# Kernel tuning notes

Hardware: AMD Instinct MI355X
Metric: run time of the kernel (lower is better)

The kernel has to match this reference:

```python
import jax, jax.numpy as jnp
import numpy as np

B, L, E, H = 2, 2048, 1024, 16
HD = E // H  # head_dim = 64
MASKED_BIAS = -10000.0


def setup_inputs() -> dict:
    key = jax.random.key(0)
    k0, k1, k2 = jax.random.split(key, 3)
    x = jax.random.normal(k0, (B, L, E), dtype=jnp.float32)
    attn_mask = jnp.zeros((B, 1, 1, L), dtype=jnp.float32)  # additive padding mask (0 = keep)
    W_in = jax.random.normal(k1, (E, 3 * E), dtype=jnp.float32) * (E ** -0.5)
    b_in = jnp.zeros((3 * E,), dtype=jnp.float32)
    W_out = jax.random.normal(k2, (E, E), dtype=jnp.float32) * (E ** -0.5)
    b_out = jnp.zeros((E,), dtype=jnp.float32)
    return {"x": x, "attn_mask": attn_mask, "W_in": W_in, "b_in": b_in,
            "W_out": W_out, "b_out": b_out}


def _split_heads(t):
    # [B, L, E] -> [B, H, L, HD]
    return t.reshape(B, L, H, HD).transpose(0, 2, 1, 3)


def reference(x, attn_mask, W_in, b_in, W_out, b_out):
    qkv = x @ W_in + b_in                      # [B, L, 3E]
    q, k, v = jnp.split(qkv, 3, axis=2)
    q, k, v = _split_heads(q), _split_heads(k), _split_heads(v)  # [B,H,L,HD]

    # Faithful to source: Q/K cast to bf16 before the score matmul.
    qb = q.astype(jnp.bfloat16)
    kb = k.astype(jnp.bfloat16)
    scores = jnp.einsum('bhqd,bhkd->bhqk', qb, kb)  # bf16 [B,H,L,L]
    scores = scores / float(HD) ** 0.5              # scale_attn_weights=True

    causal = jnp.tril(jnp.ones((L, L), dtype=bool))  # [L, L]
    scores = jnp.where(causal, scores, MASKED_BIAS)  # stays bf16
    # Adding the fp32 attn_mask promotes scores to fp32 (matches torch promotion).
    scores = scores + attn_mask                      # [B,H,L,L] fp32

    attn = jax.nn.softmax(scores, axis=-1)           # fp32, this is _attn_weights
    out = jnp.einsum('bhqk,bhkd->bhqd', attn, v)     # [B,H,L,HD]

    out = out.transpose(0, 2, 1, 3).reshape(B, L, E)  # merge heads
    out = out @ W_out + b_out                         # [B, L, E]
    return (out, attn)
```

## Files before the change

kernel.cpp:

```cpp
#include <hip/hip_runtime.h>


#define B_ 2
#define L_ 2048
#define E_ 1024
#define H_ 16
#define HD_ 64
#define M_FIX 16.0f

typedef __attribute__((ext_vector_type(8))) __bf16 bf16x8;
typedef __attribute__((ext_vector_type(4))) __bf16 bf16x4;
typedef __attribute__((ext_vector_type(4))) float f32x4;

typedef __attribute__((address_space(1))) const void gvoid_t;
typedef __attribute__((address_space(3))) void lvoid_t;

__device__ __forceinline__ void g2l16(const void* g, void* l) {
  __builtin_amdgcn_global_load_lds((gvoid_t*)g, (lvoid_t*)l, 16, 0, 0);
}

__device__ __forceinline__ f32x4 mfma16(bf16x8 a, bf16x8 b, f32x4 c) {
  return __builtin_amdgcn_mfma_f32_16x16x32_bf16(a, b, c, 0, 0, 0);
}

__global__ __launch_bounds__(256) void f32_to_bf16_vec(
    const float* __restrict__ in, __bf16* __restrict__ out, int n) {
  int i = (blockIdx.x * blockDim.x + threadIdx.x) * 4;
  if (i >= n) return;
  float4 v = *(const float4*)(in + i);
  bf16x4 o = {(__bf16)v.x, (__bf16)v.y, (__bf16)v.z, (__bf16)v.w};
  *(bf16x4*)(out + i) = o;
}

__global__ __launch_bounds__(256) void transpose_to_bf16(
    const float* __restrict__ in, __bf16* __restrict__ out, int R, int C) {
  __shared__ __bf16 tile[32][33];
  int c0 = blockIdx.x * 32, r0 = blockIdx.y * 32;
  int tx = threadIdx.x, ty = threadIdx.y;
  for (int i = ty; i < 32; i += 8)
    tile[i][tx] = (__bf16)in[(size_t)(r0 + i) * C + c0 + tx];
  __syncthreads();
  for (int i = ty; i < 32; i += 8)
    out[(size_t)(c0 + i) * R + r0 + tx] = tile[tx][i];
}

__global__ __launch_bounds__(256) void gemm_bf16_k(
    const __bf16* __restrict__ A, const __bf16* __restrict__ Bt,
    const float* __restrict__ bias, int M, int N, int K, int mode,
    float* __restrict__ outF, __bf16* __restrict__ Qb,
    __bf16* __restrict__ Kb, __bf16* __restrict__ Vt) {
  const f32x4 fz = {0.f, 0.f, 0.f, 0.f};
  int n0 = blockIdx.x * 128, m0 = blockIdx.y * 128;
  int w = threadIdx.x >> 6, l = threadIdx.x & 63;
  int wr = w >> 1, wc = w & 1, lr = l & 15, lg = l >> 4;
  __shared__ __bf16 Al[128 * 64];
  __shared__ __bf16 Bl[128 * 64];
  f32x4 acc[4][4];
#pragma unroll
  for (int i = 0; i < 4; ++i)
#pragma unroll
    for (int j = 0; j < 4; ++j) acc[i][j] = fz;

  for (int k0 = 0; k0 < K; k0 += 64) {
    __syncthreads();
#pragma unroll
    for (int i = 0; i < 4; ++i) {
      int base = (w * 4 + i) * 1024;
      int boff = base + l * 16;
      int row = boff >> 7, ch = (boff >> 4) & 7;
      g2l16(A + (size_t)(m0 + row) * K + k0 + ch * 8, (char*)Al + base);
      g2l16(Bt + (size_t)(n0 + row) * K + k0 + ch * 8, (char*)Bl + base);
    }
    __syncthreads();
    bf16x8 af[2][4], bfr[2][4];
#pragma unroll
    for (int ks = 0; ks < 2; ++ks)
#pragma unroll
      for (int f = 0; f < 4; ++f) {
        af[ks][f]  = *(const bf16x8*)&Al[(wr * 64 + f * 16 + lr) * 64 + ks * 32 + lg * 8];
        bfr[ks][f] = *(const bf16x8*)&Bl[(wc * 64 + f * 16 + lr) * 64 + ks * 32 + lg * 8];
      }
#pragma unroll
    for (int ks = 0; ks < 2; ++ks)
#pragma unroll
      for (int mf = 0; mf < 4; ++mf)
#pragma unroll
        for (int nf = 0; nf < 4; ++nf)
          acc[mf][nf] = mfma16(af[ks][mf], bfr[ks][nf], acc[mf][nf]);
  }

#pragma unroll
  for (int mf = 0; mf < 4; ++mf)
#pragma unroll
    for (int nf = 0; nf < 4; ++nf) {
      int ncol = n0 + wc * 64 + nf * 16 + lr;
      float bv = bias[ncol];
      int mr0 = m0 + wr * 64 + mf * 16 + lg * 4;
      if (mode == 1) {
#pragma unroll
        for (int jj = 0; jj < 4; ++jj)
          outF[(size_t)(mr0 + jj) * N + ncol] = acc[mf][nf][jj] + bv;
      } else {
        int reg = ncol >> 10, nn = ncol & 1023;
        int hh = nn >> 6, dd = nn & 63;
        int bb = mr0 >> 11, lp = mr0 & 2047;
        size_t bh = (size_t)bb * H_ + hh;
        if (reg == 2) {
          bf16x4 vv = {(__bf16)(acc[mf][nf][0] + bv), (__bf16)(acc[mf][nf][1] + bv),
                       (__bf16)(acc[mf][nf][2] + bv), (__bf16)(acc[mf][nf][3] + bv)};
          *(bf16x4*)&Vt[(bh * HD_ + dd) * L_ + lp] = vv;
        } else {
          __bf16* dst = (reg == 0) ? Qb : Kb;
#pragma unroll
          for (int jj = 0; jj < 4; ++jj)
            dst[(bh * L_ + lp + jj) * HD_ + dd] = (__bf16)(acc[mf][nf][jj] + bv);
        }
      }
    }
}

__global__ __launch_bounds__(256) void attn_fused3(
    const __bf16* __restrict__ Qb, const __bf16* __restrict__ Kb,
    const __bf16* __restrict__ Vt, const float* __restrict__ amask,
    float* __restrict__ attn_out, __bf16* __restrict__ merged) {
  const f32x4 fz = {0.f, 0.f, 0.f, 0.f};
  int id = blockIdx.x;
  int bh = id & 31;
  int qt = 15 - (id >> 5);
  int b = bh >> 4, h = bh & 15;
  int w = threadIdx.x >> 6, l = threadIdx.x & 63;
  int lr = l & 15, lg = l >> 4;
  const __bf16* Qh = Qb + (size_t)bh * L_ * HD_;
  const char* Kc = (const char*)(Kb + (size_t)bh * L_ * HD_);
  const char* Vc = (const char*)(Vt + (size_t)bh * HD_ * L_);
  float* attn = attn_out + (size_t)bh * L_ * L_;
  const float* mb = amask + (size_t)b * L_;

  __shared__ __bf16 Kl[2][64 * 64];
  __shared__ __bf16 Vl[2][64 * 64];
  __shared__ __bf16 Pl[4][32 * 64];
  __shared__ float Ml[L_];

  {
    int t = threadIdx.x;
    *(f32x4*)&Ml[t * 8] = *(const f32x4*)&mb[t * 8];
    *(f32x4*)&Ml[t * 8 + 4] = *(const f32x4*)&mb[t * 8 + 4];
  }

  int r0 = qt * 128 + w * 32 + lr;
  int r1 = r0 + 16;
  int ncc = 2 * qt + 2;

  bf16x8 qA0 = *(const bf16x8*)&Qh[(size_t)r0 * HD_ + lg * 8];
  bf16x8 qA1 = *(const bf16x8*)&Qh[(size_t)r0 * HD_ + 32 + lg * 8];
  bf16x8 qB0 = *(const bf16x8*)&Qh[(size_t)r1 * HD_ + lg * 8];
  bf16x8 qB1 = *(const bf16x8*)&Qh[(size_t)r1 * HD_ + 32 + lg * 8];

  auto stageK = [&](int c, int buf) {
#pragma unroll
    for (int i = 0; i < 2; ++i) {
      int seg = w * 2 + i;
      int grow = seg * 8 + (l >> 3);
      int sc8 = (l & 7) ^ (grow & 7);
      g2l16(Kc + (size_t)c * 8192 + grow * 128 + sc8 * 16,
            (char*)&Kl[buf][0] + seg * 1024);
    }
  };
  auto stageV = [&](int c, int buf) {
#pragma unroll
    for (int i = 0; i < 2; ++i) {
      int seg = w * 2 + i;
      int grow = seg * 8 + (l >> 3);
      int sc8 = (l & 7) ^ (grow & 7);
      g2l16(Vc + (size_t)grow * 4096 + (size_t)c * 128 + sc8 * 16,
            (char*)&Vl[buf][0] + seg * 1024);
    }
  };
  auto readS = [&](const __bf16* base, int row, int hf) -> bf16x8 {
    int c8 = (hf * 4 + lg) ^ (row & 7);
    return *(const bf16x8*)((const char*)base + row * 128 + c8 * 16);
  };
  auto writeP = [&](int ri, int cf, const bf16x4& v) {
    int c8 = (cf * 2 + (lg >> 1)) ^ (ri & 7);
    *(bf16x4*)((char*)&Pl[w][0] + ri * 128 + c8 * 16 + (lg & 1) * 8) = v;
  };
  auto readP = [&](int ri, int hf) -> bf16x8 {
    int c8 = (hf * 4 + lg) ^ (ri & 7);
    return *(const bf16x8*)((const char*)&Pl[w][0] + ri * 128 + c8 * 16);
  };

  float lA = 0.f, lB = 0.f;
  stageK(0, 0);
  __syncthreads();
  int cur = 0;
  for (int c = 0; c < ncc; ++c) {
    if (c + 1 < ncc) stageK(c + 1, cur ^ 1);
    f32x4 aA[4], aB[4];
#pragma unroll
    for (int cf = 0; cf < 4; ++cf) {
      bf16x8 k0 = readS(Kl[cur], cf * 16 + lr, 0);
      bf16x8 k1 = readS(Kl[cur], cf * 16 + lr, 1);
      aA[cf] = mfma16(k0, qA0, fz);
      aA[cf] = mfma16(k1, qA1, aA[cf]);
      aB[cf] = mfma16(k0, qB0, fz);
      aB[cf] = mfma16(k1, qB1, aB[cf]);
    }
    float sa = 0.f, sb = 0.f;
#pragma unroll
    for (int cf = 0; cf < 4; ++cf) {
      f32x4 mk = *(const f32x4*)&Ml[c * 64 + cf * 16 + lg * 4];
#pragma unroll
      for (int jj = 0; jj < 4; ++jj) {
        int col = c * 64 + cf * 16 + lg * 4 + jj;
        float svA = (float)(__bf16)aA[cf][jj] * 0.125f;
        if (col > r0) svA = -9984.0f;
        sa += __expf(svA + mk[jj] - M_FIX);
        float svB = (float)(__bf16)aB[cf][jj] * 0.125f;
        if (col > r1) svB = -9984.0f;
        sb += __expf(svB + mk[jj] - M_FIX);
      }
    }
    lA += sa;
    lB += sb;
    __syncthreads();
    cur ^= 1;
  }
  lA += __shfl_xor(lA, 16, 64);
  lA += __shfl_xor(lA, 32, 64);
  lB += __shfl_xor(lB, 16, 64);
  lB += __shfl_xor(lB, 32, 64);
  float liA = 1.0f / lA, liB = 1.0f / lB;

  f32x4 oA[4] = {fz, fz, fz, fz};
  f32x4 oB[4] = {fz, fz, fz, fz};
  stageK(0, 0);
  stageV(0, 0);
  __syncthreads();
  cur = 0;
  for (int c = 0; c < ncc; ++c) {
    if (c + 1 < ncc) {
      stageK(c + 1, cur ^ 1);
      stageV(c + 1, cur ^ 1);
    }
    asm volatile("" ::: "memory");
    f32x4 aA[4], aB[4];
#pragma unroll
    for (int cf = 0; cf < 4; ++cf) {
      bf16x8 k0 = readS(Kl[cur], cf * 16 + lr, 0);
      bf16x8 k1 = readS(Kl[cur], cf * 16 + lr, 1);
      aA[cf] = mfma16(k0, qA0, fz);
      aA[cf] = mfma16(k1, qA1, aA[cf]);
      aB[cf] = mfma16(k0, qB0, fz);
      aB[cf] = mfma16(k1, qB1, aB[cf]);
    }
#pragma unroll
    for (int cf = 0; cf < 4; ++cf) {
      f32x4 mk = *(const f32x4*)&Ml[c * 64 + cf * 16 + lg * 4];
      f32x4 pA, pB;
#pragma unroll
      for (int jj = 0; jj < 4; ++jj) {
        int col = c * 64 + cf * 16 + lg * 4 + jj;
        float svA = (float)(__bf16)aA[cf][jj] * 0.125f;
        if (col > r0) svA = -9984.0f;
        pA[jj] = __expf(svA + mk[jj] - M_FIX) * liA;
        float svB = (float)(__bf16)aB[cf][jj] * 0.125f;
        if (col > r1) svB = -9984.0f;
        pB[jj] = __expf(svB + mk[jj] - M_FIX) * liB;
      }
      *(f32x4*)&attn[(size_t)r0 * L_ + c * 64 + cf * 16 + lg * 4] = pA;
      *(f32x4*)&attn[(size_t)r1 * L_ + c * 64 + cf * 16 + lg * 4] = pB;
      bf16x4 ha = {(__bf16)pA[0], (__bf16)pA[1], (__bf16)pA[2], (__bf16)pA[3]};
      bf16x4 hb = {(__bf16)pB[0], (__bf16)pB[1], (__bf16)pB[2], (__bf16)pB[3]};
      writeP(lr, cf, ha);
      writeP(16 + lr, cf, hb);
    }
    bf16x8 pA0 = readP(lr, 0), pA1 = readP(lr, 1);
    bf16x8 pB0 = readP(16 + lr, 0), pB1 = readP(16 + lr, 1);
#pragma unroll
    for (int dt = 0; dt < 4; ++dt) {
      bf16x8 v0 = readS(Vl[cur], dt * 16 + lr, 0);
      bf16x8 v1 = readS(Vl[cur], dt * 16 + lr, 1);
      oA[dt] = mfma16(v0, pA0, oA[dt]);
      oA[dt] = mfma16(v1, pA1, oA[dt]);
      oB[dt] = mfma16(v0, pB0, oB[dt]);
      oB[dt] = mfma16(v1, pB1, oB[dt]);
    }
    asm volatile("s_waitcnt vmcnt(8)" ::: "memory");
    __builtin_amdgcn_s_barrier();
    __builtin_amdgcn_sched_barrier(0);
    cur ^= 1;
  }

#pragma unroll
  for (int dt = 0; dt < 4; ++dt) {
    bf16x4 oa = {(__bf16)oA[dt][0], (__bf16)oA[dt][1], (__bf16)oA[dt][2],
                 (__bf16)oA[dt][3]};
    bf16x4 ob = {(__bf16)oB[dt][0], (__bf16)oB[dt][1], (__bf16)oB[dt][2],
                 (__bf16)oB[dt][3]};
    *(bf16x4*)&merged[((size_t)b * L_ + r0) * E_ + h * HD_ + dt * 16 + lg * 4] = oa;
    *(bf16x4*)&merged[((size_t)b * L_ + r1) * E_ + h * HD_ + dt * 16 + lg * 4] = ob;
  }

  for (int c = ncc; c < 32; ++c)
#pragma unroll
    for (int q = 0; q < 4; ++q) {
      *(f32x4*)&attn[(size_t)r0 * L_ + c * 64 + q * 16 + lg * 4] = fz;
      *(f32x4*)&attn[(size_t)r1 * L_ + c * 64 + q * 16 + lg * 4] = fz;
    }
}

extern "C" void kernel_launch(void* const* d_in, const int* in_sizes, int n_in,
                              void* d_out, int out_size, void* d_ws,
                              size_t ws_size, hipStream_t stream) {
  const float* x     = (const float*)d_in[0];
  const float* amask = (const float*)d_in[1];
  const float* W_in  = (const float*)d_in[2];
  const float* b_in  = (const float*)d_in[3];
  const float* W_out = (const float*)d_in[4];
  const float* b_out = (const float*)d_in[5];

  float* out  = (float*)d_out;
  float* attn = out + (size_t)B_ * L_ * E_;

  char* ws = (char*)d_ws;
  __bf16* xb     = (__bf16*)(ws + 0);
  __bf16* WtIn   = (__bf16*)(ws + 8388608);
  __bf16* WtOut  = (__bf16*)(ws + 14680064);
  __bf16* Qb     = (__bf16*)(ws + 16777216);
  __bf16* Kb     = (__bf16*)(ws + 25165824);
  __bf16* Vt     = (__bf16*)(ws + 33554432);
  __bf16* merged = (__bf16*)(ws + 41943040);

  int nx = B_ * L_ * E_;
  f32_to_bf16_vec<<<nx / (256 * 4), 256, 0, stream>>>(x, xb, nx);
  transpose_to_bf16<<<dim3(3 * E_ / 32, E_ / 32), dim3(32, 8), 0, stream>>>(
      W_in, WtIn, E_, 3 * E_);
  transpose_to_bf16<<<dim3(E_ / 32, E_ / 32), dim3(32, 8), 0, stream>>>(
      W_out, WtOut, E_, E_);

  gemm_bf16_k<<<dim3(3 * E_ / 128, B_ * L_ / 128), 256, 0, stream>>>(
      xb, WtIn, b_in, B_ * L_, 3 * E_, E_, 0, nullptr, Qb, Kb, Vt);

  attn_fused3<<<16 * 32, 256, 0, stream>>>(Qb, Kb, Vt, amask, attn, merged);

  gemm_bf16_k<<<dim3(E_ / 128, B_ * L_ / 128), 256, 0, stream>>>(
      merged, WtOut, b_out, B_ * L_, E_, E_, 1, out, nullptr, nullptr,
      nullptr);
}
```

Measured before the change: 286.1 us.

## Split attention over key range into two halves and double-buffer GEMM staging

After: 330.5 us. +15.5%, slower.

```diff
diff --git a/kernel.cpp b/kernel.cpp
--- a/kernel.cpp
+++ b/kernel.cpp
@@ -53,32 +53,41 @@
   int n0 = blockIdx.x * 128, m0 = blockIdx.y * 128;
   int w = threadIdx.x >> 6, l = threadIdx.x & 63;
   int wr = w >> 1, wc = w & 1, lr = l & 15, lg = l >> 4;
-  __shared__ __bf16 Al[128 * 64];
-  __shared__ __bf16 Bl[128 * 64];
+  __shared__ __bf16 Al[2][128 * 64];
+  __shared__ __bf16 Bl[2][128 * 64];
   f32x4 acc[4][4];
 #pragma unroll
   for (int i = 0; i < 4; ++i)
 #pragma unroll
     for (int j = 0; j < 4; ++j) acc[i][j] = fz;
 
-  for (int k0 = 0; k0 < K; k0 += 64) {
-    __syncthreads();
+  auto stage = [&](int k0, int buf) {
 #pragma unroll
     for (int i = 0; i < 4; ++i) {
       int base = (w * 4 + i) * 1024;
       int boff = base + l * 16;
       int row = boff >> 7, ch = (boff >> 4) & 7;
-      g2l16(A + (size_t)(m0 + row) * K + k0 + ch * 8, (char*)Al + base);
-      g2l16(Bt + (size_t)(n0 + row) * K + k0 + ch * 8, (char*)Bl + base);
-    }
-    __syncthreads();
+      g2l16(A + (size_t)(m0 + row) * K + k0 + ch * 8, (char*)&Al[buf][0] + base);
+      g2l16(Bt + (size_t)(n0 + row) * K + k0 + ch * 8, (char*)&Bl[buf][0] + base);
+    }
+  };
+
+  int nk = K >> 6;
+  stage(0, 0);
+  asm volatile("s_waitcnt vmcnt(0)" ::: "memory");
+  __builtin_amdgcn_s_barrier();
+  __builtin_amdgcn_sched_barrier(0);
+  int cur = 0;
+  for (int t = 0; t < nk; ++t) {
+    if (t + 1 < nk) stage((t + 1) << 6, cur ^ 1);
+    asm volatile("" ::: "memory");
     bf16x8 af[2][4], bfr[2][4];
 #pragma unroll
     for (int ks = 0; ks < 2; ++ks)
 #pragma unroll
       for (int f = 0; f < 4; ++f) {
-        af[ks][f]  = *(const bf16x8*)&Al[(wr * 64 + f * 16 + lr) * 64 + ks * 32 + lg * 8];
-        bfr[ks][f] = *(const bf16x8*)&Bl[(wc * 64 + f * 16 + lr) * 64 + ks * 32 + lg * 8];
+        af[ks][f]  = *(const bf16x8*)&Al[cur][(wr * 64 + f * 16 + lr) * 64 + ks * 32 + lg * 8];
+        bfr[ks][f] = *(const bf16x8*)&Bl[cur][(wc * 64 + f * 16 + lr) * 64 + ks * 32 + lg * 8];
       }
 #pragma unroll
     for (int ks = 0; ks < 2; ++ks)
@@ -87,6 +96,10 @@
 #pragma unroll
         for (int nf = 0; nf < 4; ++nf)
           acc[mf][nf] = mfma16(af[ks][mf], bfr[ks][nf], acc[mf][nf]);
+    asm volatile("s_waitcnt vmcnt(0)" ::: "memory");
+    __builtin_amdgcn_s_barrier();
+    __builtin_amdgcn_sched_barrier(0);
+    cur ^= 1;
   }
 
 #pragma unroll
@@ -119,37 +132,27 @@
     }
 }
 
-__global__ __launch_bounds__(256) void attn_fused3(
+__global__ __launch_bounds__(256) void attn_p1(
     const __bf16* __restrict__ Qb, const __bf16* __restrict__ Kb,
-    const __bf16* __restrict__ Vt, const float* __restrict__ amask,
-    float* __restrict__ attn_out, __bf16* __restrict__ merged) {
+    const float* __restrict__ amask, float* __restrict__ lpart) {
   const f32x4 fz = {0.f, 0.f, 0.f, 0.f};
   int id = blockIdx.x;
   int bh = id & 31;
-  int qt = 15 - (id >> 5);
-  int b = bh >> 4, h = bh & 15;
+  int t = id >> 5;
+  int qt = 15 - (t >> 1);
+  int ph = t & 1;
+  int b = bh >> 4;
   int w = threadIdx.x >> 6, l = threadIdx.x & 63;
   int lr = l & 15, lg = l >> 4;
   const __bf16* Qh = Qb + (size_t)bh * L_ * HD_;
   const char* Kc = (const char*)(Kb + (size_t)bh * L_ * HD_);
-  const char* Vc = (const char*)(Vt + (size_t)bh * HD_ * L_);
-  float* attn = attn_out + (size_t)bh * L_ * L_;
   const float* mb = amask + (size_t)b * L_;
 
   __shared__ __bf16 Kl[2][64 * 64];
-  __shared__ __bf16 Vl[2][64 * 64];
-  __shared__ __bf16 Pl[4][32 * 64];
-  __shared__ float Ml[L_];
-
-  {
-    int t = threadIdx.x;
-    *(f32x4*)&Ml[t * 8] = *(const f32x4*)&mb[t * 8];
-    *(f32x4*)&Ml[t * 8 + 4] = *(const f32x4*)&mb[t * 8 + 4];
-  }
 
   int r0 = qt * 128 + w * 32 + lr;
   int r1 = r0 + 16;
-  int ncc = 2 * qt + 2;
+  int c0 = ph * (qt + 1), c1 = c0 + qt + 1;
 
   bf16x8 qA0 = *(const bf16x8*)&Qh[(size_t)r0 * HD_ + lg * 8];
   bf16x8 qA1 = *(const bf16x8*)&Qh[(size_t)r0 * HD_ + 32 + lg * 8];
@@ -166,35 +169,17 @@
             (char*)&Kl[buf][0] + seg * 1024);
     }
   };
-  auto stageV = [&](int c, int buf) {
-#pragma unroll
-    for (int i = 0; i < 2; ++i) {
-      int seg = w * 2 + i;
-      int grow = seg * 8 + (l >> 3);
-      int sc8 = (l & 7) ^ (grow & 7);
-      g2l16(Vc + (size_t)grow * 4096 + (size_t)c * 128 + sc8 * 16,
-            (char*)&Vl[buf][0] + seg * 1024);
-    }
-  };
   auto readS = [&](const __bf16* base, int row, int hf) -> bf16x8 {
     int c8 = (hf * 4 + lg) ^ (row & 7);
     return *(const bf16x8*)((const char*)base + row * 128 + c8 * 16);
   };
-  auto writeP = [&](int ri, int cf, const bf16x4& v) {
-    int c8 = (cf * 2 + (lg >> 1)) ^ (ri & 7);
-    *(bf16x4*)((char*)&Pl[w][0] + ri * 128 + c8 * 16 + (lg & 1) * 8) = v;
-  };
-  auto readP = [&](int ri, int hf) -> bf16x8 {
-    int c8 = (hf * 4 + lg) ^ (ri & 7);
-    return *(const bf16x8*)((const char*)&Pl[w][0] + ri * 128 + c8 * 16);
-  };
 
   float lA = 0.f, lB = 0.f;
-  stageK(0, 0);
+  stageK(c0, 0);
   __syncthreads();
   int cur = 0;
-  for (int c = 0; c < ncc; ++c) {
-    if (c + 1 < ncc) stageK(c + 1, cur ^ 1);
+  for (int c = c0; c < c1; ++c) {
+    if (c + 1 < c1) stageK(c + 1, cur ^ 1);
     f32x4 aA[4], aB[4];
 #pragma unroll
     for (int cf = 0; cf < 4; ++cf) {
@@ -208,7 +193,7 @@
     float sa = 0.f, sb = 0.f;
 #pragma unroll
     for (int cf = 0; cf < 4; ++cf) {
-      f32x4 mk = *(const f32x4*)&Ml[c * 64 + cf * 16 + lg * 4];
+      f32x4 mk = *(const f32x4*)&mb[c * 64 + cf * 16 + lg * 4];
 #pragma unroll
       for (int jj = 0; jj < 4; ++jj) {
         int col = c * 64 + cf * 16 + lg * 4 + jj;
@@ -229,16 +214,92 @@
   lA += __shfl_xor(lA, 32, 64);
   lB += __shfl_xor(lB, 16, 64);
   lB += __shfl_xor(lB, 32, 64);
-  float liA = 1.0f / lA, liB = 1.0f / lB;
+  if (lg == 0) {
+    lpart[ph * (B_ * H_ * L_) + bh * L_ + r0] = lA;
+    lpart[ph * (B_ * H_ * L_) + bh * L_ + r1] = lB;
+  }
+}
+
+__global__ __launch_bounds__(256) void attn_p2(
+    const __bf16* __restrict__ Qb, const __bf16* __restrict__ Kb,
+    const __bf16* __restrict__ Vt, const float* __restrict__ amask,
+    const float* __restrict__ lpart, float* __restrict__ attn_out,
+    __bf16* __restrict__ op0, __bf16* __restrict__ op1) {
+  const f32x4 fz = {0.f, 0.f, 0.f, 0.f};
+  int id = blockIdx.x;
+  int bh = id & 31;
+  int t = id >> 5;
+  int qt = 15 - (t >> 1);
+  int ph = t & 1;
+  int b = bh >> 4, h = bh & 15;
+  int w = threadIdx.x >> 6, l = threadIdx.x & 63;
+  int lr = l & 15, lg = l >> 4;
+  const __bf16* Qh = Qb + (size_t)bh * L_ * HD_;
+  const char* Kc = (const char*)(Kb + (size_t)bh * L_ * HD_);
+  const char* Vc = (const char*)(Vt + (size_t)bh * HD_ * L_);
+  float* attn = attn_out + (size_t)bh * L_ * L_;
+  const float* mb = amask + (size_t)b * L_;
+  __bf16* opart = ph ? op1 : op0;
+
+  __shared__ __bf16 Kl[2][64 * 64];
+  __shared__ __bf16 Vl[2][64 * 64];
+  __shared__ __bf16 Pl[4][32 * 64];
+
+  int r0 = qt * 128 + w * 32 + lr;
+  int r1 = r0 + 16;
+  int c0 = ph * (qt + 1), c1 = c0 + qt + 1;
+
+  float liA = 1.0f / (lpart[bh * L_ + r0] + lpart[B_ * H_ * L_ + bh * L_ + r0]);
+  float liB = 1.0f / (lpart[bh * L_ + r1] + lpart[B_ * H_ * L_ + bh * L_ + r1]);
+
+  bf16x8 qA0 = *(const bf16x8*)&Qh[(size_t)r0 * HD_ + lg * 8];
+  bf16x8 qA1 = *(const bf16x8*)&Qh[(size_t)r0 * HD_ + 32 + lg * 8];
+  bf16x8 qB0 = *(const bf16x8*)&Qh[(size_t)r1 * HD_ + lg * 8];
+  bf16x8 qB1 = *(const bf16x8*)&Qh[(size_t)r1 * HD_ + 32 + lg * 8];
+
+  auto stageK = [&](int c, int buf) {
+#pragma unroll
+    for (int i = 0; i < 2; ++i) {
+      int seg = w * 2 + i;
+      int grow = seg * 8 + (l >> 3);
+      int sc8 = (l & 7) ^ (grow & 7);
+      g2l16(Kc + (size_t)c * 8192 + grow * 128 + sc8 * 16,
+            (char*)&Kl[buf][0] + seg * 1024);
+    }
+  };
+  auto stageV = [&](int c, int buf) {
+#pragma unroll
+    for (int i = 0; i < 2; ++i) {
+      int seg = w * 2 + i;
+      int grow = seg * 8 + (l >> 3);
+      int sc8 = (l & 7) ^ (grow & 7);
+      g2l16(Vc + (size_t)grow * 4096 + (size_t)c * 128 + sc8 * 16,
+            (char*)&Vl[buf][0] + seg * 1024);
+    }
+  };
+  auto readS = [&](const __bf16* base, int row, int hf) -> bf16x8 {
+    int c8 = (hf * 4 + lg) ^ (row & 7);
+    return *(const bf16x8*)((const char*)base + row * 128 + c8 * 16);
+  };
+  auto writeP = [&](int ri, int cf, const bf16x4& v) {
+    int c8 = (cf * 2 + (lg >> 1)) ^ (ri & 7);
+    *(bf16x4*)((char*)&Pl[w][0] + ri * 128 + c8 * 16 + (lg & 1) * 8) = v;
+  };
+  auto readP = [&](int ri, int hf) -> bf16x8 {
+    int c8 = (hf * 4 + lg) ^ (ri & 7);
+    return *(const bf16x8*)((const char*)&Pl[w][0] + ri * 128 + c8 * 16);
+  };
 
   f32x4 oA[4] = {fz, fz, fz, fz};
   f32x4 oB[4] = {fz, fz, fz, fz};
-  stageK(0, 0);
-  stageV(0, 0);
-  __syncthreads();
-  cur = 0;
-  for (int c = 0; c < ncc; ++c) {
-    if (c + 1 < ncc) {
+  stageK(c0, 0);
+  stageV(c0, 0);
+  asm volatile("s_waitcnt vmcnt(0)" ::: "memory");
+  __builtin_amdgcn_s_barrier();
+  __builtin_amdgcn_sched_barrier(0);
+  int cur = 0;
+  for (int c = c0; c < c1; ++c) {
+    if (c + 1 < c1) {
       stageK(c + 1, cur ^ 1);
       stageV(c + 1, cur ^ 1);
     }
@@ -255,7 +316,7 @@
     }
 #pragma unroll
     for (int cf = 0; cf < 4; ++cf) {
-      f32x4 mk = *(const f32x4*)&Ml[c * 64 + cf * 16 + lg * 4];
+      f32x4 mk = *(const f32x4*)&mb[c * 64 + cf * 16 + lg * 4];
       f32x4 pA, pB;
 #pragma unroll
       for (int jj = 0; jj < 4; ++jj) {
@@ -297,16 +358,30 @@
                  (__bf16)oA[dt][3]};
     bf16x4 ob = {(__bf16)oB[dt][0], (__bf16)oB[dt][1], (__bf16)oB[dt][2],
                  (__bf16)oB[dt][3]};
-    *(bf16x4*)&merged[((size_t)b * L_ + r0) * E_ + h * HD_ + dt * 16 + lg * 4] = oa;
-    *(bf16x4*)&merged[((size_t)b * L_ + r1) * E_ + h * HD_ + dt * 16 + lg * 4] = ob;
+    *(bf16x4*)&opart[((size_t)b * L_ + r0) * E_ + h * HD_ + dt * 16 + lg * 4] = oa;
+    *(bf16x4*)&opart[((size_t)b * L_ + r1) * E_ + h * HD_ + dt * 16 + lg * 4] = ob;
   }
 
-  for (int c = ncc; c < 32; ++c)
-#pragma unroll
-    for (int q = 0; q < 4; ++q) {
-      *(f32x4*)&attn[(size_t)r0 * L_ + c * 64 + q * 16 + lg * 4] = fz;
-      *(f32x4*)&attn[(size_t)r1 * L_ + c * 64 + q * 16 + lg * 4] = fz;
-    }
+  if (ph == 1)
+    for (int c = 2 * qt + 2; c < 32; ++c)
+#pragma unroll
+      for (int q = 0; q < 4; ++q) {
+        *(f32x4*)&attn[(size_t)r0 * L_ + c * 64 + q * 16 + lg * 4] = fz;
+        *(f32x4*)&attn[(size_t)r1 * L_ + c * 64 + q * 16 + lg * 4] = fz;
+      }
+}
+
+__global__ __launch_bounds__(256) void attn_reduce(
+    const __bf16* __restrict__ a, const __bf16* __restrict__ b,
+    __bf16* __restrict__ m, int n) {
+  int i = (blockIdx.x * 256 + threadIdx.x) * 8;
+  if (i >= n) return;
+  bf16x8 va = *(const bf16x8*)&a[i];
+  bf16x8 vb = *(const bf16x8*)&b[i];
+  bf16x8 o;
+#pragma unroll
+  for (int j = 0; j < 8; ++j) o[j] = (__bf16)((float)va[j] + (float)vb[j]);
+  *(bf16x8*)&m[i] = o;
 }
 
 extern "C" void kernel_launch(void* const* d_in, const int* in_sizes, int n_in,
@@ -330,6 +405,10 @@
   __bf16* Kb     = (__bf16*)(ws + 25165824);
   __bf16* Vt     = (__bf16*)(ws + 33554432);
   __bf16* merged = (__bf16*)(ws + 41943040);
+  float*  lpart  = (float*)(ws + 50331648);
+
+  __bf16* op0 = (__bf16*)d_out;
+  __bf16* op1 = (__bf16*)((char*)d_out + 8388608);
 
   int nx = B_ * L_ * E_;
   f32_to_bf16_vec<<<nx / (256 * 4), 256, 0, stream>>>(x, xb, nx);
@@ -341,7 +420,10 @@
   gemm_bf16_k<<<dim3(3 * E_ / 128, B_ * L_ / 128), 256, 0, stream>>>(
       xb, WtIn, b_in, B_ * L_, 3 * E_, E_, 0, nullptr, Qb, Kb, Vt);
 
-  attn_fused3<<<16 * 32, 256, 0, stream>>>(Qb, Kb, Vt, amask, attn, merged);
+  attn_p1<<<32 * 32, 256, 0, stream>>>(Qb, Kb, amask, lpart);
+  attn_p2<<<32 * 32, 256, 0, stream>>>(Qb, Kb, Vt, amask, lpart, attn, op0,
+                                       op1);
+  attn_reduce<<<nx / (256 * 8), 256, 0, stream>>>(op0, op1, merged, nx);
 
   gemm_bf16_k<<<dim3(E_ / 128, B_ * L_ / 128), 256, 0, stream>>>(
       merged, WtOut, b_out, B_ * L_, E_, E_, 1, out, nullptr, nullptr,
```
